# Kernel tuning notes

Hardware: AMD Instinct MI355X
Metric: run time of the kernel (lower is better)

Reference implementation:

```python
import jax, jax.numpy as jnp
import numpy as np

B, N, L, S, H, E, D = 4, 32, 256, 256, 8, 64, 64

def setup_inputs() -> dict:
    key = jax.random.key(0)
    k1, k2, k3, k4 = jax.random.split(key, 4)
    queries = jax.random.normal(k1, (B, N, L, H, E), dtype=jnp.float32)
    keys = jax.random.normal(k2, (B, N, S, H, E), dtype=jnp.float32)
    values = jax.random.normal(k3, (B, N, S, H, D), dtype=jnp.float32)
    # additive causal mask [L, S]: 0 where allowed, -1e9 where masked
    causal = jnp.tril(jnp.ones((L, S), dtype=bool))
    attn_mask = jnp.where(causal, 0.0, -1e9).astype(jnp.float32)
    # cross-layer accumulated prior scores [B, N, H, L, S]
    attn_scores = jax.random.normal(k4, (B, N, H, L, S), dtype=jnp.float32) * 0.1
    query_lengths = jnp.full((B,), L, dtype=jnp.int32)
    key_lengths = jnp.full((B,), S, dtype=jnp.int32)
    return {"queries": queries, "keys": keys, "values": values,
            "attn_mask": attn_mask, "attn_scores": attn_scores,
            "query_lengths": query_lengths, "key_lengths": key_lengths}

def reference(queries, keys, values, attn_mask, attn_scores, query_lengths, key_lengths):
    # queries: [B,N,L,H,E], keys: [B,N,S,H,E], values: [B,N,S,H,D]
    e = queries.shape[-1]
    softmax_temp = 1.0 / np.sqrt(e).astype(np.float32)
    QK = jnp.einsum('bnlhe,bnshe->bnhls', queries, keys)
    # additive mask broadcast over [B,N,H]
    scores = QK + attn_mask + attn_scores  # accumulated scores returned for next layer
    A = jax.nn.softmax(softmax_temp * scores, axis=-1)  # dropout omitted (eval mode)
    V = jnp.einsum('bnhls,bnshd->bnlhd', A, values)
    return scores, V
```

## Files before the change

kernel.cpp:

```cpp
#include <hip/hip_runtime.h>
#include <stdint.h>


typedef __attribute__((ext_vector_type(8))) short bfrag;
typedef __attribute__((ext_vector_type(4))) float f32x4;
typedef __attribute__((ext_vector_type(4))) int i32x4;

__device__ __forceinline__ uint32_t f2bf(float f) {
  uint32_t u = __builtin_bit_cast(uint32_t, f);
  return (u + 0x7FFFu + ((u >> 16) & 1u)) >> 16;
}
__device__ __forceinline__ uint32_t pk(float a, float b) {
  return f2bf(a) | (f2bf(b) << 16);
}

#define MFMA(a, b, c) __builtin_amdgcn_mfma_f32_16x16x32_bf16((a), (b), (c), 0, 0, 0)

__global__ __launch_bounds__(1024, 2) void attn_kernel(
    const float* __restrict__ Qg, const float* __restrict__ Kg,
    const float* __restrict__ Vg, const float* __restrict__ Pg,
    float* __restrict__ Sc, float* __restrict__ Ov)
{
  __shared__ char Kb[2][8192];
  __shared__ char Vb[2][8192];

  const int bnh = blockIdx.x;
  const int bn = bnh >> 3, h = bnh & 7;
  const int t = threadIdx.x;
  const int lane = t & 63;
  const int wave = t >> 6;
  const int ql = lane & 15;
  const int g  = lane >> 4;
  const int qt = (int)((0x783C96D25A1EB4F0ull >> (wave * 4)) & 15);
  const int q = qt * 16 + ql;
  const int pvmax = qt >> 2;
  const int swz = (ql & 7) << 4;
  const float temp = 0.125f;

  const int kr_ = t >> 4;
  const int kc4 = (t & 15) * 4;
  const int vd_ = t & 63;
  const int vs4 = (t >> 6) * 4;
  const float* kgp = Kg + (size_t)bn * 131072 + h * 64 + (size_t)kr_ * 512 + kc4;
  const float* vgp = Vg + (size_t)bn * 131072 + h * 64 + (size_t)vs4 * 512 + vd_;
  const int kwoff = (kr_ * 128 + kc4 * 2) ^ ((kr_ & 7) << 4);
  const int vwoff = (vd_ * 128 + vs4 * 2) ^ ((vd_ & 7) << 4);

  f32x4 kreg = *(const f32x4*)kgp;
  float vr0 = vgp[0], vr1 = vgp[512], vr2 = vgp[1024], vr3 = vgp[1536];
  {
    uint2 kk; kk.x = pk(kreg[0], kreg[1]); kk.y = pk(kreg[2], kreg[3]);
    *(uint2*)(&Kb[0][0] + kwoff) = kk;
    uint2 vv; vv.x = pk(vr0, vr1); vv.y = pk(vr2, vr3);
    *(uint2*)(&Vb[0][0] + vwoff) = vv;
  }
  kreg = *(const f32x4*)(kgp + 32768);
  vr0 = vgp[32768]; vr1 = vgp[32768 + 512];
  vr2 = vgp[32768 + 1024]; vr3 = vgp[32768 + 1536];

  bfrag qf[2];
#pragma unroll
  for (int ks = 0; ks < 2; ++ks) {
    const float* qp = Qg + (size_t)bn * 131072 + (size_t)q * 512 + h * 64 + ks * 32 + g * 8;
    const f32x4 qa = *(const f32x4*)qp;
    const f32x4 qb = *(const f32x4*)(qp + 4);
    union { i32x4 i; bfrag b; } u;
    u.i = i32x4{(int)pk(qa.x, qa.y), (int)pk(qa.z, qa.w),
                (int)pk(qb.x, qb.y), (int)pk(qb.z, qb.w)};
    qf[ks] = u.b;
  }

  f32x4 O[4];
#pragma unroll
  for (int ds = 0; ds < 4; ++ds) O[ds] = f32x4{0.f, 0.f, 0.f, 0.f};
  float m = -1e30f, lsum = 0.f;

  const size_t scb = (size_t)bnh << 16;
  const float* prp = Pg + scb + (size_t)q * 256 + 4 * g;
  float* scp = Sc + scb + (size_t)q * 256 + 4 * g;

  f32x4 pr[4];
#pragma unroll
  for (int j = 0; j < 4; ++j)
    pr[j] = __builtin_nontemporal_load((const f32x4*)(prp + 16 * j));

  asm volatile("s_waitcnt lgkmcnt(0)" ::: "memory");
  __builtin_amdgcn_s_barrier();

#pragma unroll 1
  for (int it = 0; it < 4; ++it) {
    const int s0 = it * 64;
    const int bp = (it & 1) << 13;
    f32x4 acc[2][2];
#pragma unroll
    for (int sub = 0; sub < 2; ++sub)
#pragma unroll
      for (int ss = 0; ss < 2; ++ss) {
        bfrag kf0 = *(const bfrag*)(&Kb[0][0] + bp +
            (((sub * 32 + 16 * ss + ql) * 128 + 0 * 64 + g * 16) ^ swz));
        bfrag kf1 = *(const bfrag*)(&Kb[0][0] + bp +
            (((sub * 32 + 16 * ss + ql) * 128 + 1 * 64 + g * 16) ^ swz));
        f32x4 a = f32x4{0.f, 0.f, 0.f, 0.f};
        a = MFMA(kf0, qf[0], a);
        a = MFMA(kf1, qf[1], a);
        const int sb = s0 + sub * 32 + 16 * ss + 4 * g;
#pragma unroll
        for (int r = 0; r < 4; ++r)
          a[r] = (sb + r <= q) ? a[r] : a[r] - 1e9f;
        acc[sub][ss] = a + pr[sub * 2 + ss];
      }

    if (it < 3) {
#pragma unroll
      for (int j = 0; j < 4; ++j)
        pr[j] = __builtin_nontemporal_load(
            (const f32x4*)(prp + (it + 1) * 64 + 16 * j));
    }

    __builtin_nontemporal_store(acc[0][0], (f32x4*)(scp + s0));
    __builtin_nontemporal_store(acc[0][1], (f32x4*)(scp + s0 + 16));
    __builtin_nontemporal_store(acc[1][0], (f32x4*)(scp + s0 + 32));
    __builtin_nontemporal_store(acc[1][1], (f32x4*)(scp + s0 + 48));

    if (it <= pvmax) {
      float tm = -1e30f;
#pragma unroll
      for (int sub = 0; sub < 2; ++sub)
#pragma unroll
        for (int ss = 0; ss < 2; ++ss)
#pragma unroll
          for (int r = 0; r < 4; ++r) tm = fmaxf(tm, acc[sub][ss][r]);
      tm = fmaxf(tm, __shfl_xor(tm, 16));
      tm = fmaxf(tm, __shfl_xor(tm, 32));
      tm *= temp;
      const float mnew = fmaxf(m, tm);
      const float fct = __expf(m - mnew);
      m = mnew;
      float pv[16];
#pragma unroll
      for (int sub = 0; sub < 2; ++sub)
#pragma unroll
        for (int ss = 0; ss < 2; ++ss)
#pragma unroll
          for (int r = 0; r < 4; ++r)
            pv[sub * 8 + ss * 4 + r] = __expf(fmaf(temp, acc[sub][ss][r], -mnew));
      float ts = 0.f;
#pragma unroll
      for (int j = 0; j < 16; ++j) ts += pv[j];
      ts += __shfl_xor(ts, 16);
      ts += __shfl_xor(ts, 32);
      lsum = lsum * fct + ts;
#pragma unroll
      for (int ds = 0; ds < 4; ++ds) O[ds] *= fct;

#pragma unroll
      for (int sub = 0; sub < 2; ++sub) {
        const int w0x = (int)pk(pv[sub * 8 + 0], pv[sub * 8 + 1]);
        const int w0y = (int)pk(pv[sub * 8 + 2], pv[sub * 8 + 3]);
        const int w1x = (int)pk(pv[sub * 8 + 4], pv[sub * 8 + 5]);
        const int w1y = (int)pk(pv[sub * 8 + 6], pv[sub * 8 + 7]);
        const int srcA = ((g & 1) << 5) + ql;
        const int a0 = __shfl(w0x, srcA),      a1 = __shfl(w1x, srcA);
        const int b0 = __shfl(w0y, srcA),      b1 = __shfl(w1y, srcA);
        const int c0 = __shfl(w0x, srcA + 16), c1 = __shfl(w1x, srcA + 16);
        const int d0 = __shfl(w0y, srcA + 16), d1 = __shfl(w1y, srcA + 16);
        union { i32x4 i; bfrag b; } pu;
        pu.i = i32x4{g < 2 ? a0 : a1, g < 2 ? b0 : b1,
                     g < 2 ? c0 : c1, g < 2 ? d0 : d1};
#pragma unroll
        for (int ds = 0; ds < 4; ++ds) {
          bfrag vf = *(const bfrag*)(&Vb[0][0] + bp +
              (((16 * ds + ql) * 128 + sub * 64 + g * 16) ^ swz));
          O[ds] = MFMA(vf, pu.b, O[ds]);
        }
      }
    }

    if (it < 3) {
      const int bp1 = ((it + 1) & 1) << 13;
      uint2 kk; kk.x = pk(kreg[0], kreg[1]); kk.y = pk(kreg[2], kreg[3]);
      *(uint2*)(&Kb[0][0] + bp1 + kwoff) = kk;
      uint2 vv; vv.x = pk(vr0, vr1); vv.y = pk(vr2, vr3);
      *(uint2*)(&Vb[0][0] + bp1 + vwoff) = vv;
      if (it < 2) {
        kreg = *(const f32x4*)(kgp + (size_t)(it + 2) * 32768);
        vr0 = vgp[(it + 2) * 32768];
        vr1 = vgp[(it + 2) * 32768 + 512];
        vr2 = vgp[(it + 2) * 32768 + 1024];
        vr3 = vgp[(it + 2) * 32768 + 1536];
      }
    }
    asm volatile("s_waitcnt lgkmcnt(0)" ::: "memory");
    __builtin_amdgcn_s_barrier();
  }

  {
    const float inv = 1.f / lsum;
    float* op = Ov + (size_t)bn * 131072 + (size_t)q * 512 + h * 64 + 4 * g;
#pragma unroll
    for (int ds = 0; ds < 4; ++ds) {
      f32x4 o = O[ds] * inv;
      *(f32x4*)(op + 16 * ds) = o;
    }
  }
}

extern "C" void kernel_launch(void* const* d_in, const int* in_sizes, int n_in,
                              void* d_out, int out_size, void* d_ws, size_t ws_size,
                              hipStream_t stream) {
  const float* Qg = (const float*)d_in[0];
  const float* Kg = (const float*)d_in[1];
  const float* Vg = (const float*)d_in[2];
  const float* Pg = (const float*)d_in[4];
  float* Sc = (float*)d_out;
  float* Ov = Sc + (size_t)4 * 32 * 8 * 256 * 256;
  attn_kernel<<<dim3(1024), dim3(1024), 0, stream>>>(Qg, Kg, Vg, Pg, Sc, Ov);
}
```

Baseline: 155.1 us.

## Load K directly from global per wave and stage all of V in LDS once

Removes the double-buffered K/V LDS pipeline and the per-iteration barriers. Each wave now reads its K fragments straight from global memory (through cache) and converts them to bf16 in registers. All 256 rows of V are transposed into a single 32KB LDS buffer up front, behind one barrier. This removes per-iteration synchronisation but means 16 waves redundantly fetch K from L2, and LDS use grows, which can hurt occupancy at 2 blocks per CU.

```diff
diff --git a/kernel.cpp b/kernel.cpp
--- a/kernel.cpp
+++ b/kernel.cpp
@@ -21,8 +21,7 @@
     const float* __restrict__ Vg, const float* __restrict__ Pg,
     float* __restrict__ Sc, float* __restrict__ Ov)
 {
-  __shared__ char Kb[2][8192];
-  __shared__ char Vb[2][8192];
+  __shared__ char Vt[64 * 512];
 
   const int bnh = blockIdx.x;
   const int bn = bnh >> 3, h = bnh & 7;
@@ -37,26 +36,22 @@
   const int swz = (ql & 7) << 4;
   const float temp = 0.125f;
 
-  const int kr_ = t >> 4;
-  const int kc4 = (t & 15) * 4;
-  const int vd_ = t & 63;
-  const int vs4 = (t >> 6) * 4;
-  const float* kgp = Kg + (size_t)bn * 131072 + h * 64 + (size_t)kr_ * 512 + kc4;
-  const float* vgp = Vg + (size_t)bn * 131072 + h * 64 + (size_t)vs4 * 512 + vd_;
-  const int kwoff = (kr_ * 128 + kc4 * 2) ^ ((kr_ & 7) << 4);
-  const int vwoff = (vd_ * 128 + vs4 * 2) ^ ((vd_ & 7) << 4);
-
-  f32x4 kreg = *(const f32x4*)kgp;
-  float vr0 = vgp[0], vr1 = vgp[512], vr2 = vgp[1024], vr3 = vgp[1536];
   {
-    uint2 kk; kk.x = pk(kreg[0], kreg[1]); kk.y = pk(kreg[2], kreg[3]);
-    *(uint2*)(&Kb[0][0] + kwoff) = kk;
-    uint2 vv; vv.x = pk(vr0, vr1); vv.y = pk(vr2, vr3);
-    *(uint2*)(&Vb[0][0] + vwoff) = vv;
-  }
-  kreg = *(const f32x4*)(kgp + 32768);
-  vr0 = vgp[32768]; vr1 = vgp[32768 + 512];
-  vr2 = vgp[32768 + 1024]; vr3 = vgp[32768 + 1536];
+    const int d = t & 63, sg = t >> 6;
+    const float* vp = Vg + (size_t)bn * 131072 + h * 64 + d;
+#pragma unroll
+    for (int it = 0; it < 4; ++it) {
+      const int sv = it * 64 + sg * 4;
+      const float v0 = vp[(size_t)(sv + 0) * 512];
+      const float v1 = vp[(size_t)(sv + 1) * 512];
+      const float v2 = vp[(size_t)(sv + 2) * 512];
+      const float v3 = vp[(size_t)(sv + 3) * 512];
+      uint2 vv;
+      vv.x = pk(v0, v1);
+      vv.y = pk(v2, v3);
+      *(uint2*)(Vt + ((d * 512 + sv * 2) ^ ((d & 7) << 4))) = vv;
+    }
+  }
 
   bfrag qf[2];
 #pragma unroll
@@ -70,6 +65,8 @@
     qf[ks] = u.b;
   }
 
+  __syncthreads();
+
   f32x4 O[4];
 #pragma unroll
   for (int ds = 0; ds < 4; ++ds) O[ds] = f32x4{0.f, 0.f, 0.f, 0.f};
@@ -78,31 +75,35 @@
   const size_t scb = (size_t)bnh << 16;
   const float* prp = Pg + scb + (size_t)q * 256 + 4 * g;
   float* scp = Sc + scb + (size_t)q * 256 + 4 * g;
+  const float* kgb = Kg + (size_t)bn * 131072 + h * 64 + g * 8;
 
   f32x4 pr[4];
 #pragma unroll
   for (int j = 0; j < 4; ++j)
     pr[j] = __builtin_nontemporal_load((const f32x4*)(prp + 16 * j));
-
-  asm volatile("s_waitcnt lgkmcnt(0)" ::: "memory");
-  __builtin_amdgcn_s_barrier();
 
 #pragma unroll 1
   for (int it = 0; it < 4; ++it) {
     const int s0 = it * 64;
-    const int bp = (it & 1) << 13;
     f32x4 acc[2][2];
 #pragma unroll
     for (int sub = 0; sub < 2; ++sub)
 #pragma unroll
       for (int ss = 0; ss < 2; ++ss) {
-        bfrag kf0 = *(const bfrag*)(&Kb[0][0] + bp +
-            (((sub * 32 + 16 * ss + ql) * 128 + 0 * 64 + g * 16) ^ swz));
-        bfrag kf1 = *(const bfrag*)(&Kb[0][0] + bp +
-            (((sub * 32 + 16 * ss + ql) * 128 + 1 * 64 + g * 16) ^ swz));
+        const int srow = s0 + sub * 32 + 16 * ss + ql;
+        const float* kp = kgb + (size_t)srow * 512;
+        const f32x4 ka = *(const f32x4*)kp;
+        const f32x4 kb = *(const f32x4*)(kp + 4);
+        const f32x4 kc = *(const f32x4*)(kp + 32);
+        const f32x4 kd = *(const f32x4*)(kp + 36);
+        union { i32x4 i; bfrag b; } u0, u1;
+        u0.i = i32x4{(int)pk(ka.x, ka.y), (int)pk(ka.z, ka.w),
+                     (int)pk(kb.x, kb.y), (int)pk(kb.z, kb.w)};
+        u1.i = i32x4{(int)pk(kc.x, kc.y), (int)pk(kc.z, kc.w),
+                     (int)pk(kd.x, kd.y), (int)pk(kd.z, kd.w)};
         f32x4 a = f32x4{0.f, 0.f, 0.f, 0.f};
-        a = MFMA(kf0, qf[0], a);
-        a = MFMA(kf1, qf[1], a);
+        a = MFMA(u0.b, qf[0], a);
+        a = MFMA(u1.b, qf[1], a);
         const int sb = s0 + sub * 32 + 16 * ss + 4 * g;
 #pragma unroll
         for (int r = 0; r < 4; ++r)
@@ -169,29 +170,12 @@
                      g < 2 ? c0 : c1, g < 2 ? d0 : d1};
 #pragma unroll
         for (int ds = 0; ds < 4; ++ds) {
-          bfrag vf = *(const bfrag*)(&Vb[0][0] + bp +
-              (((16 * ds + ql) * 128 + sub * 64 + g * 16) ^ swz));
+          bfrag vf = *(const bfrag*)(Vt +
+              (((16 * ds + ql) * 512 + (s0 + sub * 32) * 2 + g * 16) ^ swz));
           O[ds] = MFMA(vf, pu.b, O[ds]);
         }
       }
     }
-
-    if (it < 3) {
-      const int bp1 = ((it + 1) & 1) << 13;
-      uint2 kk; kk.x = pk(kreg[0], kreg[1]); kk.y = pk(kreg[2], kreg[3]);
-      *(uint2*)(&Kb[0][0] + bp1 + kwoff) = kk;
-      uint2 vv; vv.x = pk(vr0, vr1); vv.y = pk(vr2, vr3);
-      *(uint2*)(&Vb[0][0] + bp1 + vwoff) = vv;
-      if (it < 2) {
-        kreg = *(const f32x4*)(kgp + (size_t)(it + 2) * 32768);
-        vr0 = vgp[(it + 2) * 32768];
-        vr1 = vgp[(it + 2) * 32768 + 512];
-        vr2 = vgp[(it + 2) * 32768 + 1024];
-        vr3 = vgp[(it + 2) * 32768 + 1536];
-      }
-    }
-    asm volatile("s_waitcnt lgkmcnt(0)" ::: "memory");
-    __builtin_amdgcn_s_barrier();
   }
 
   {
```

Measured after the change: 234.6 us. +51.2%, slower.
